# Optimization experiments

Hardware: AMD Instinct MI355X
Metric: run time of the kernel (lower is better)

Reference implementation:

```python
import jax, jax.numpy as jnp
import numpy as np
import math

# token_types from init_kwargs: ordered ranges [start, end)
TYPE_STARTS = jnp.array([0, 128, 256, 512, 1024], dtype=jnp.int64)
TYPE_ENDS = jnp.array([128, 256, 512, 1024, 2048], dtype=jnp.int64)
VOCAB = 2048
D_MODEL = 512
EPS = 1e-5


def setup_inputs() -> dict:
    key = jax.random.key(0)
    k1, k2, k3 = jax.random.split(key, 3)
    x = jax.random.randint(k1, (16, 4096), 0, VOCAB, dtype=jnp.int64)
    # init like the torch module: normal with std sqrt(2/(d-8)) and sqrt(2/8)
    token_emb_table = jax.random.normal(k2, (VOCAB, D_MODEL - 8), dtype=jnp.float32) * math.sqrt(2.0 / (D_MODEL - 8))
    type_emb_table = jax.random.normal(k3, (5, 8), dtype=jnp.float32) * math.sqrt(2.0 / 8)
    ln_gamma = jnp.ones((D_MODEL,), dtype=jnp.float32)
    ln_beta = jnp.zeros((D_MODEL,), dtype=jnp.float32)
    return {"x": x, "token_emb_table": token_emb_table, "type_emb_table": type_emb_table,
            "ln_gamma": ln_gamma, "ln_beta": ln_beta}


def _type_indices(x):
    # first type whose [start, end) contains the token; 0 if none (argmax of
    # all-False mask is 0, matching the torch fallback `return 0`).
    matches = (x[..., None] >= TYPE_STARTS) & (x[..., None] < TYPE_ENDS)  # [B,S,T]
    return jnp.argmax(matches, axis=-1)


def reference(x, token_emb_table, type_emb_table, ln_gamma, ln_beta):
    token_emb = token_emb_table[x]                    # [B,S,d_model-8]
    type_emb = type_emb_table[_type_indices(x)]       # [B,S,8]
    combined = jnp.concatenate([token_emb, type_emb], axis=-1)  # [B,S,d_model]
    mean = jnp.mean(combined, axis=-1, keepdims=True)
    var = jnp.var(combined, axis=-1, keepdims=True)
    normed = (combined - mean) * jax.lax.rsqrt(var + EPS) * ln_gamma + ln_beta
    # dropout is identity in eval mode
    return normed * jnp.asarray(math.sqrt(D_MODEL), dtype=normed.dtype)
```

## Files before the change

kernel.cpp:

```cpp
#include <hip/hip_runtime.h>

#define D_MODEL 512
#define D_TOK   504
#define EPS     1e-5f
#define SQRT_D  22.627416997969522f

typedef float f32x4 __attribute__((ext_vector_type(4)));

__global__ __launch_bounds__(256) void musical_emb_kernel(
    const int*   __restrict__ x,
    const float* __restrict__ tok_tab,
    const float* __restrict__ typ_tab,
    const float* __restrict__ gamma,
    const float* __restrict__ beta,
    float*       __restrict__ out,
    int n_tokens)
{
    const int wave = (int)((blockIdx.x * blockDim.x + threadIdx.x) >> 6);
    const int lane = (int)(threadIdx.x & 63);
    if (wave >= n_tokens) return;

    const int xi = x[wave];
    const int t = (xi >= 128) + (xi >= 256) + (xi >= 512) + (xi >= 1024);

    const size_t offA = (size_t)lane * 4;
    const size_t offB = 256 + (size_t)lane * 4;

    const float4 a = *reinterpret_cast<const float4*>(tok_tab + (size_t)xi * D_TOK + offA);

    const float* pB = tok_tab + (size_t)xi * D_TOK + offB;
    const float* pT = typ_tab + (size_t)t * 8 + (size_t)(lane - 62) * 4;
    const float4 b = *reinterpret_cast<const float4*>((lane >= 62) ? pT : pB);

    float s  = a.x + a.y + a.z + a.w + b.x + b.y + b.z + b.w;
    float s2 = a.x * a.x + a.y * a.y + a.z * a.z + a.w * a.w
             + b.x * b.x + b.y * b.y + b.z * b.z + b.w * b.w;

#pragma unroll
    for (int off = 32; off > 0; off >>= 1) {
        s  += __shfl_xor(s,  off, 64);
        s2 += __shfl_xor(s2, off, 64);
    }

    const float inv_n = 1.0f / (float)D_MODEL;
    const float mean  = s * inv_n;
    const float var   = s2 * inv_n - mean * mean;
    const float rs    = rsqrtf(var + EPS) * SQRT_D;

    const float4 g0 = *reinterpret_cast<const float4*>(gamma + offA);
    const float4 g1 = *reinterpret_cast<const float4*>(gamma + offB);
    const float4 b0 = *reinterpret_cast<const float4*>(beta  + offA);
    const float4 b1 = *reinterpret_cast<const float4*>(beta  + offB);

    f32x4 o0, o1;
    o0.x = (a.x - mean) * rs * g0.x + b0.x * SQRT_D;
    o0.y = (a.y - mean) * rs * g0.y + b0.y * SQRT_D;
    o0.z = (a.z - mean) * rs * g0.z + b0.z * SQRT_D;
    o0.w = (a.w - mean) * rs * g0.w + b0.w * SQRT_D;
    o1.x = (b.x - mean) * rs * g1.x + b1.x * SQRT_D;
    o1.y = (b.y - mean) * rs * g1.y + b1.y * SQRT_D;
    o1.z = (b.z - mean) * rs * g1.z + b1.z * SQRT_D;
    o1.w = (b.w - mean) * rs * g1.w + b1.w * SQRT_D;

    float* orow = out + (size_t)wave * D_MODEL;
    __builtin_nontemporal_store(o0, reinterpret_cast<f32x4*>(orow + offA));
    __builtin_nontemporal_store(o1, reinterpret_cast<f32x4*>(orow + offB));
}

extern "C" void kernel_launch(void* const* d_in, const int* in_sizes, int n_in,
                              void* d_out, int out_size, void* d_ws, size_t ws_size,
                              hipStream_t stream) {
    const int*   x       = (const int*)d_in[0];
    const float* tok_tab = (const float*)d_in[1];
    const float* typ_tab = (const float*)d_in[2];
    const float* gamma   = (const float*)d_in[3];
    const float* beta    = (const float*)d_in[4];
    float*       out     = (float*)d_out;

    const int n_tokens = in_sizes[0];
    const int threads  = 256;
    const int blocks   = (n_tokens * 64 + threads - 1) / threads;

    musical_emb_kernel<<<blocks, threads, 0, stream>>>(
        x, tok_tab, typ_tab, gamma, beta, out, n_tokens);
}
```

Measured before the change: 28.77 us.

## Process four tokens per wave with double-buffered gather prefetch

Adds a kernel in which each wave handles four tokens strided by the total wave count. Gamma and beta (prescaled by sqrt(d)) are loaded once per wave, and the next token's row gather is issued before the current token is reduced and normalized. The aim is to spread per-wave setup over more tokens and hide gather latency. The cost is more registers per thread and a quarter as many blocks, and the new path is only used when the token count exactly equals 65536, otherwise the original kernel runs.

```diff
diff --git a/kernel.cpp b/kernel.cpp
--- a/kernel.cpp
+++ b/kernel.cpp
@@ -5,7 +5,99 @@
 #define EPS     1e-5f
 #define SQRT_D  22.627416997969522f
 
+#define NBLK  4096
+#define WPB   4
+#define NWAVE (NBLK * WPB)
+#define ITER  4
+
 typedef float f32x4 __attribute__((ext_vector_type(4)));
+
+__global__ __launch_bounds__(256) void fused_pipe_kernel(
+    const int*   __restrict__ x,
+    const float* __restrict__ tok_tab,
+    const float* __restrict__ typ_tab,
+    const float* __restrict__ gamma,
+    const float* __restrict__ beta,
+    float*       __restrict__ out)
+{
+    const int wave = (int)(blockIdx.x * WPB + (threadIdx.x >> 6));
+    const int lane = (int)(threadIdx.x & 63);
+
+    const size_t offA = (size_t)lane * 4;
+    const size_t offB = 256 + (size_t)lane * 4;
+
+    const float4 g0  = *reinterpret_cast<const float4*>(gamma + offA);
+    const float4 g1  = *reinterpret_cast<const float4*>(gamma + offB);
+    const float4 bb0 = *reinterpret_cast<const float4*>(beta + offA);
+    const float4 bb1 = *reinterpret_cast<const float4*>(beta + offB);
+    const float4 bs0 = make_float4(bb0.x * SQRT_D, bb0.y * SQRT_D, bb0.z * SQRT_D, bb0.w * SQRT_D);
+    const float4 bs1 = make_float4(bb1.x * SQRT_D, bb1.y * SQRT_D, bb1.z * SQRT_D, bb1.w * SQRT_D);
+
+    int id[ITER];
+#pragma unroll
+    for (int j = 0; j < ITER; ++j)
+        id[j] = x[wave + j * NWAVE];
+#pragma unroll
+    for (int j = 0; j < ITER; ++j)
+        id[j] = __builtin_amdgcn_readfirstlane(id[j]);
+
+    auto ptrA = [&](int xi) -> const float* {
+        return tok_tab + (size_t)xi * D_TOK + offA;
+    };
+    auto ptrB = [&](int xi) -> const float* {
+        const int t = (xi >= 128) + (xi >= 256) + (xi >= 512) + (xi >= 1024);
+        const float* pB = tok_tab + (size_t)xi * D_TOK + offB;
+        const float* pT = typ_tab + (size_t)t * 8 + (size_t)(lane - 62) * 4;
+        return (lane >= 62) ? pT : pB;
+    };
+
+    float4 aA, bA, aB, bB;
+    aA = *reinterpret_cast<const float4*>(ptrA(id[0]));
+    bA = *reinterpret_cast<const float4*>(ptrB(id[0]));
+
+#pragma unroll
+    for (int j = 0; j < ITER; ++j) {
+        if (j + 1 < ITER) {
+            if ((j & 1) == 0) {
+                aB = *reinterpret_cast<const float4*>(ptrA(id[j + 1]));
+                bB = *reinterpret_cast<const float4*>(ptrB(id[j + 1]));
+            } else {
+                aA = *reinterpret_cast<const float4*>(ptrA(id[j + 1]));
+                bA = *reinterpret_cast<const float4*>(ptrB(id[j + 1]));
+            }
+        }
+        const float4 a = ((j & 1) == 0) ? aA : aB;
+        const float4 b = ((j & 1) == 0) ? bA : bB;
+
+        float s  = a.x + a.y + a.z + a.w + b.x + b.y + b.z + b.w;
+        float s2 = a.x * a.x + a.y * a.y + a.z * a.z + a.w * a.w
+                 + b.x * b.x + b.y * b.y + b.z * b.z + b.w * b.w;
+#pragma unroll
+        for (int off = 32; off > 0; off >>= 1) {
+            s  += __shfl_xor(s,  off, 64);
+            s2 += __shfl_xor(s2, off, 64);
+        }
+
+        const float inv_n = 1.0f / (float)D_MODEL;
+        const float mean  = s * inv_n;
+        const float var   = s2 * inv_n - mean * mean;
+        const float rs    = rsqrtf(var + EPS) * SQRT_D;
+
+        f32x4 o0, o1;
+        o0.x = (a.x - mean) * rs * g0.x + bs0.x;
+        o0.y = (a.y - mean) * rs * g0.y + bs0.y;
+        o0.z = (a.z - mean) * rs * g0.z + bs0.z;
+        o0.w = (a.w - mean) * rs * g0.w + bs0.w;
+        o1.x = (b.x - mean) * rs * g1.x + bs1.x;
+        o1.y = (b.y - mean) * rs * g1.y + bs1.y;
+        o1.z = (b.z - mean) * rs * g1.z + bs1.z;
+        o1.w = (b.w - mean) * rs * g1.w + bs1.w;
+
+        float* orow = out + (size_t)(wave + j * NWAVE) * D_MODEL;
+        __builtin_nontemporal_store(o0, reinterpret_cast<f32x4*>(orow + offA));
+        __builtin_nontemporal_store(o1, reinterpret_cast<f32x4*>(orow + offB));
+    }
+}
 
 __global__ __launch_bounds__(256) void musical_emb_kernel(
     const int*   __restrict__ x,
@@ -27,7 +119,6 @@
     const size_t offB = 256 + (size_t)lane * 4;
 
     const float4 a = *reinterpret_cast<const float4*>(tok_tab + (size_t)xi * D_TOK + offA);
-
     const float* pB = tok_tab + (size_t)xi * D_TOK + offB;
     const float* pT = typ_tab + (size_t)t * 8 + (size_t)(lane - 62) * 4;
     const float4 b = *reinterpret_cast<const float4*>((lane >= 62) ? pT : pB);
@@ -78,9 +169,12 @@
     float*       out     = (float*)d_out;
 
     const int n_tokens = in_sizes[0];
-    const int threads  = 256;
-    const int blocks   = (n_tokens * 64 + threads - 1) / threads;
 
-    musical_emb_kernel<<<blocks, threads, 0, stream>>>(
-        x, tok_tab, typ_tab, gamma, beta, out, n_tokens);
+    if (n_tokens == NWAVE * ITER) {
+        fused_pipe_kernel<<<NBLK, 256, 0, stream>>>(
+            x, tok_tab, typ_tab, gamma, beta, out);
+    } else {
+        musical_emb_kernel<<<(n_tokens * 64 + 255) / 256, 256, 0, stream>>>(
+            x, tok_tab, typ_tab, gamma, beta, out, n_tokens);
+    }
 }
```

Result: slower. 35.35 us (+22.9%).
